# Optimization experiments

Hardware: AMD Instinct MI355X
Metric: run time of the kernel (lower is better)

## Reference

```python
import jax, jax.numpy as jnp
import numpy as np

B, N, DIM, H, HD, COND, BS = 2, 1024, 768, 12, 64, 128, 16
S = 2 * N  # noised tokens [0:N) concatenated with clean x0 tokens [N:2N)
EPS = 1e-5
NEG = -1e30


def setup_inputs() -> dict:
    key = jax.random.key(0)
    ks = jax.random.split(key, 8)
    d = {}
    d['x'] = jax.random.normal(ks[0], (B, S, DIM), jnp.float32)
    d['c'] = jax.random.normal(ks[1], (B, COND), jnp.float32)
    # Rotary table for positions 0..N-1 (each half of the 2N sequence reuses the same positions)
    inv_freq = 1.0 / (10000.0 ** (np.arange(0, HD, 2, dtype=np.float64) / HD))
    freqs = np.arange(N, dtype=np.float64)[:, None] * inv_freq[None, :]
    emb = np.concatenate([freqs, freqs], axis=-1)  # [N, HD]
    cos = np.tile(np.cos(emb), (2, 1))[None, :, None, None, :]
    sin = np.tile(np.sin(emb), (2, 1))[None, :, None, None, :]
    d['cos'] = jnp.asarray(cos, jnp.float32)
    d['sin'] = jnp.asarray(sin, jnp.float32)
    # block-causal diffusion mask (flex_attention_mask): same (block, x0-flag) OR
    # cross-attention from noised block q>0 to strictly earlier CLEAN (x0) blocks
    idx = np.arange(S)
    fl = (idx >= N).astype(np.int64)
    blk = np.where(fl == 1, (idx - N) // BS, idx // BS)
    same = (blk[:, None] == blk[None, :]) & (fl[:, None] == fl[None, :])
    allowed = (blk[:, None] > 0) & (blk[None, :] < blk[:, None]) & (fl[None, :] == 1)
    d['mask'] = jnp.asarray(same | allowed)
    # parameters (adaLN is zero-init in the source; randomized here so the block is non-trivial)
    w = 0.02
    d['norm1_w'] = jnp.ones((DIM,), jnp.float32)
    d['qkv_w'] = jax.random.normal(ks[2], (3 * DIM, DIM), jnp.float32) * w
    d['attn_out_w'] = jax.random.normal(ks[3], (DIM, DIM), jnp.float32) * w
    d['norm2_w'] = jnp.ones((DIM,), jnp.float32)
    d['mlp_w1'] = jax.random.normal(ks[4], (4 * DIM, DIM), jnp.float32) * w
    d['mlp_b1'] = jnp.zeros((4 * DIM,), jnp.float32)
    d['mlp_w2'] = jax.random.normal(ks[5], (DIM, 4 * DIM), jnp.float32) * w
    d['mlp_b2'] = jnp.zeros((DIM,), jnp.float32)
    d['adaLN_w'] = jax.random.normal(ks[6], (6 * DIM, COND), jnp.float32) * w
    d['adaLN_b'] = jax.random.normal(ks[7], (6 * DIM,), jnp.float32) * w
    return d


def _ln(x, w):
    # F.layer_norm (no bias) followed by learned scale, as in the custom LayerNorm
    mu = x.mean(-1, keepdims=True)
    xc = x - mu
    var = (xc * xc).mean(-1, keepdims=True)
    return xc * jax.lax.rsqrt(var + EPS) * w


def reference(x, c, cos, sin, mask, norm1_w, qkv_w, attn_out_w, norm2_w,
              mlp_w1, mlp_b1, mlp_w2, mlp_b2, adaLN_w, adaLN_b):
    # adaLN modulation: [B, 6*DIM] -> six [B, 1, DIM] chunks
    mods = c @ adaLN_w.T + adaLN_b
    (shift_msa, scale_msa, gate_msa,
     shift_mlp, scale_mlp, gate_mlp) = jnp.split(mods[:, None, :], 6, axis=-1)
    x_skip = x
    h = _ln(x, norm1_w) * (1.0 + scale_msa) + shift_msa  # modulate_fused
    # qkv projection + rotary (torchscript path: qkv*cos + rotate_half(qkv)*sin)
    qkv = (h @ qkv_w.T).reshape(x.shape[0], S, 3, H, HD)
    rot = jnp.concatenate([-qkv[..., HD // 2:], qkv[..., :HD // 2]], axis=-1)
    qkv = qkv * cos + rot * sin
    q, k, v = qkv[:, :, 0], qkv[:, :, 1], qkv[:, :, 2]
    # SDPA with the block-causal diffusion mask, scale 1/sqrt(head_dim)
    scores = jnp.einsum('bqhd,bkhd->bhqk', q, k) / np.sqrt(HD).astype(np.float32)
    scores = jnp.where(mask[None, None], scores, NEG)
    p = jax.nn.softmax(scores, axis=-1)
    a = jnp.einsum('bhqk,bkhd->bqhd', p, v).reshape(x.shape[0], S, DIM)
    # bias_dropout_add_scale (inference => no dropout): gate * attn_out + residual
    x = gate_msa * (a @ attn_out_w.T) + x_skip
    h2 = _ln(x, norm2_w) * (1.0 + scale_mlp) + shift_mlp
    m = jax.nn.gelu(h2 @ mlp_w1.T + mlp_b1, approximate=True) @ mlp_w2.T + mlp_b2
    return x + gate_mlp * m
```

## Files before the change

### kernel.cpp

```cpp
#include <hip/hip_runtime.h>
#include <hip/hip_bf16.h>

#define EPS 1e-5f

typedef __attribute__((ext_vector_type(8))) short bf16x8;
typedef __attribute__((ext_vector_type(4))) short bf16x4;
typedef __attribute__((ext_vector_type(4))) float f32x4;

__device__ __forceinline__ f32x4 mfma_bf16(bf16x8 a, bf16x8 b, f32x4 c) {
    return __builtin_amdgcn_mfma_f32_16x16x32_bf16(a, b, c, 0, 0, 0);
}

__device__ __forceinline__ void async_ld16(const void* g, void* l) {
    __builtin_amdgcn_global_load_lds(
        (const __attribute__((address_space(1))) void*)g,
        (__attribute__((address_space(3))) void*)l, 16, 0, 0);
}

__global__ void k_adaln(const float* __restrict__ c, const float* __restrict__ w,
                        const float* __restrict__ bias, float* __restrict__ mods) {
    int i = blockIdx.x * 256 + threadIdx.x;
    int b = i / 4608, row = i - b * 4608;
    const float4* cv = (const float4*)(c + b * 128);
    const float4* wv = (const float4*)(w + (long)row * 128);
    float acc = 0.f;
#pragma unroll
    for (int k = 0; k < 32; ++k) {
        float4 a = cv[k], bb = wv[k];
        acc += a.x * bb.x + a.y * bb.y + a.z * bb.z + a.w * bb.w;
    }
    mods[i] = acc + bias[row];
}

__global__ void k_f2b4(const float* __restrict__ a, __hip_bfloat16* __restrict__ oa, int na,
                       const float* __restrict__ b, __hip_bfloat16* __restrict__ ob, int nb,
                       const float* __restrict__ c, __hip_bfloat16* __restrict__ oc, int nc,
                       const float* __restrict__ d, __hip_bfloat16* __restrict__ od, int nd) {
    int i = blockIdx.x * 256 + threadIdx.x;
    if (i < na) { oa[i] = __float2bfloat16(a[i]); return; }
    i -= na;
    if (i < nb) { ob[i] = __float2bfloat16(b[i]); return; }
    i -= nb;
    if (i < nc) { oc[i] = __float2bfloat16(c[i]); return; }
    i -= nc;
    if (i < nd) od[i] = __float2bfloat16(d[i]);
}

__global__ void k_ln_mod(const float* __restrict__ x, const float* __restrict__ w,
                         const float* __restrict__ mods, int shiftOff, int scaleOff,
                         __hip_bfloat16* __restrict__ out) {
    int token = blockIdx.x;
    int lane = threadIdx.x;
    const float4* xr = (const float4*)(x + (long)token * 768);
    float4 v0 = xr[lane], v1 = xr[lane + 64], v2 = xr[lane + 128];
    float s  = v0.x + v0.y + v0.z + v0.w + v1.x + v1.y + v1.z + v1.w + v2.x + v2.y + v2.z + v2.w;
    float ss = v0.x*v0.x + v0.y*v0.y + v0.z*v0.z + v0.w*v0.w
             + v1.x*v1.x + v1.y*v1.y + v1.z*v1.z + v1.w*v1.w
             + v2.x*v2.x + v2.y*v2.y + v2.z*v2.z + v2.w*v2.w;
#pragma unroll
    for (int m = 32; m >= 1; m >>= 1) { s += __shfl_xor(s, m); ss += __shfl_xor(ss, m); }
    float mu = s * (1.f / 768.f);
    float var = ss * (1.f / 768.f) - mu * mu;
    float rs = rsqrtf(var + EPS);
    int b = token >> 11;
    const float* sh = mods + b * 4608 + shiftOff;
    const float* sc = mods + b * 4608 + scaleOff;
    __hip_bfloat16* o = out + (long)token * 768;
    float4 vv[3] = {v0, v1, v2};
#pragma unroll
    for (int kk = 0; kk < 3; ++kk) {
        int cbase = (lane + 64 * kk) * 4;
        const float* p = (const float*)&vv[kk];
#pragma unroll
        for (int j = 0; j < 4; ++j) {
            int col = cbase + j;
            float hv = (p[j] - mu) * rs * w[col] * (1.f + sc[col]) + sh[col];
            o[col] = __float2bfloat16(hv);
        }
    }
}

__global__ __launch_bounds__(256) void k_attn(
    const __hip_bfloat16* __restrict__ q, const __hip_bfloat16* __restrict__ k,
    const __hip_bfloat16* __restrict__ vT, __hip_bfloat16* __restrict__ out) {
    __shared__ __hip_bfloat16 pbuf[4][640];
    int wave = threadIdx.x >> 6;
    int lane = threadIdx.x & 63;
    int l15 = lane & 15, quad = lane >> 4;
    int bh = blockIdx.x >> 5;
    int pp = blockIdx.x & 31;
    int fl, blk;
    if      (wave == 0) { fl = 0; blk = 2 * pp; }
    else if (wave == 1) { fl = 0; blk = 2 * pp + 1; }
    else if (wave == 2) { fl = 1; blk = 63 - 2 * pp; }
    else                { fl = 1; blk = 62 - 2 * pp; }
    int qblk = fl * 64 + blk;

    const __hip_bfloat16* Q = q + ((long)bh * 2048 + qblk * 16) * 64;
    bf16x8 qa = *(const bf16x8*)(Q + l15 * 64 + quad * 8);
    bf16x8 qb = *(const bf16x8*)(Q + l15 * 64 + 32 + quad * 8);
    const __hip_bfloat16* K = k + (long)bh * 2048 * 64;
    const __hip_bfloat16* V = vT + (long)bh * 64 * 2048;
    __hip_bfloat16* P = &pbuf[wave][0];

    const f32x4 vzero = {0.f, 0.f, 0.f, 0.f};
    f32x4 o[4]; float l[4];
#pragma unroll
    for (int r = 0; r < 4; ++r) { o[r] = vzero; l[r] = 0.f; }

    int plen = (blk + fl) * 16;
    int nch = (plen + 31) >> 5;
    int total = nch + (fl ? 0 : 1);

    int kbase = (0 < nch) ? 1024 : blk * 16;
    bool v1 = (0 < nch) && (16 < plen);
    bf16x8 ka, kb, k1a, k1b;
    {
        const __hip_bfloat16* K0 = K + (long)kbase * 64;
        ka = *(const bf16x8*)(K0 + l15 * 64 + quad * 8);
        kb = *(const bf16x8*)(K0 + l15 * 64 + 32 + quad * 8);
        k1a = ka; k1b = kb;
        if (v1) {
            const __hip_bfloat16* K1 = K0 + 16 * 64;
            k1a = *(const bf16x8*)(K1 + l15 * 64 + quad * 8);
            k1b = *(const bf16x8*)(K1 + l15 * 64 + 32 + quad * 8);
        }
    }

    for (int ci = 0; ci < total; ++ci) {
        bf16x8 vf[4];
#pragma unroll
        for (int tt = 0; tt < 4; ++tt)
            vf[tt] = *(const bf16x8*)(V + (long)(tt * 16 + l15) * 2048 + kbase + quad * 8);

        f32x4 s0 = mfma_bf16(qb, kb, mfma_bf16(qa, ka, vzero));
        f32x4 s1 = vzero;
        if (v1) s1 = mfma_bf16(qb, k1b, mfma_bf16(qa, k1a, vzero));

        bool hasNext = (ci + 1) < total;
        int nkbase = kbase; bool nv1 = false;
        bf16x8 nka = ka, nkb = kb, nk1a = ka, nk1b = kb;
        if (hasNext) {
            nkbase = (ci + 1 < nch) ? 1024 + (ci + 1) * 32 : blk * 16;
            nv1 = (ci + 1 < nch) && ((ci + 1) * 32 + 16) < plen;
            const __hip_bfloat16* K0 = K + (long)nkbase * 64;
            nka = *(const bf16x8*)(K0 + l15 * 64 + quad * 8);
            nkb = *(const bf16x8*)(K0 + l15 * 64 + 32 + quad * 8);
            if (nv1) {
                const __hip_bfloat16* K1 = K0 + 16 * 64;
                nk1a = *(const bf16x8*)(K1 + l15 * 64 + quad * 8);
                nk1b = *(const bf16x8*)(K1 + l15 * 64 + 32 + quad * 8);
            }
        }

        float p0[4], p1[4];
#pragma unroll
        for (int r = 0; r < 4; ++r) p0[r] = __expf(s0[r]);
        if (v1) {
#pragma unroll
            for (int r = 0; r < 4; ++r) p1[r] = __expf(s1[r]);
        } else {
#pragma unroll
            for (int r = 0; r < 4; ++r) p1[r] = 0.f;
        }
#pragma unroll
        for (int r = 0; r < 4; ++r) {
            l[r] += p0[r] + p1[r];
            int row = quad * 4 + r;
            P[row * 36 + l15]      = __float2bfloat16(p0[r]);
            P[row * 36 + 16 + l15] = __float2bfloat16(p1[r]);
        }
        asm volatile("s_waitcnt lgkmcnt(0)" ::: "memory");
        union { bf16x4 h[2]; bf16x8 v; } u;
        u.h[0] = *(const bf16x4*)(P + l15 * 36 + quad * 8);
        u.h[1] = *(const bf16x4*)(P + l15 * 36 + quad * 8 + 4);
        bf16x8 pa = u.v;
#pragma unroll
        for (int tt = 0; tt < 4; ++tt) o[tt] = mfma_bf16(pa, vf[tt], o[tt]);
        asm volatile("s_waitcnt lgkmcnt(0)" ::: "memory");

        kbase = nkbase; v1 = nv1;
        ka = nka; kb = nkb; k1a = nk1a; k1b = nk1b;
    }

    int b = bh / 12, h = bh - b * 12;
    int seqbase = qblk * 16;
#pragma unroll
    for (int r = 0; r < 4; ++r) {
        float lr = l[r];
#pragma unroll
        for (int msk = 1; msk < 16; msk <<= 1) lr += __shfl_xor(lr, msk, 16);
        float inv = 1.f / lr;
        long row = b * 2048 + seqbase + quad * 4 + r;
#pragma unroll
        for (int tt = 0; tt < 4; ++tt)
            out[row * 768 + h * 64 + tt * 16 + l15] = __float2bfloat16(o[tt][r] * inv);
    }
}

template <int MODE, int TN>
__global__ __launch_bounds__(TN == 128 ? 256 : 128) void k_gemm(
    const __hip_bfloat16* __restrict__ A, const __hip_bfloat16* __restrict__ W,
    float* __restrict__ Cf, __hip_bfloat16* __restrict__ Cb,
    const float* __restrict__ bias, const float* __restrict__ mods, int gateOff,
    const float* __restrict__ resid, const float* __restrict__ cosb,
    const float* __restrict__ sinb, __hip_bfloat16* __restrict__ qo,
    __hip_bfloat16* __restrict__ ko, __hip_bfloat16* __restrict__ vo,
    int M, int N, int K) {
    constexpr int NW = (TN == 128) ? 4 : 2;
    constexpr int ACH = 512 / (NW * 64);
    constexpr int BCH = (TN * 4) / (NW * 64);
    constexpr int NINST = ACH + BCH;
    __shared__ __hip_bfloat16 lA[3][128 * 32];
    __shared__ __hip_bfloat16 lB[3][TN * 32];
    int t = threadIdx.x;
    int wave = t >> 6, lane = t & 63, l15 = lane & 15, quad = lane >> 4;
    int wr = (TN == 128) ? (wave >> 1) : wave;
    int wc = (TN == 128) ? (wave & 1) : 0;
    int sw8 = (quad ^ ((l15 >> 1) & 3)) * 8;
    long bm = blockIdx.x, bn = blockIdx.y;
    const __hip_bfloat16* Ab = A + bm * 128 * K;
    const __hip_bfloat16* Wb = W + bn * TN * K;

    long soffA[ACH], soffB[BCH];
#pragma unroll
    for (int cc = 0; cc < ACH; ++cc) {
        int chunk = cc * NW * 64 + t;
        int row = chunk >> 2;
        int c = (chunk & 3) ^ ((row >> 1) & 3);
        soffA[cc] = (long)row * K + c * 8;
    }
#pragma unroll
    for (int cc = 0; cc < BCH; ++cc) {
        int chunk = cc * NW * 64 + t;
        int row = chunk >> 2;
        int c = (chunk & 3) ^ ((row >> 1) & 3);
        soffB[cc] = (long)row * K + c * 8;
    }
    auto stage = [&](int k0, int buf) {
        char* lAc = (char*)&lA[buf][0];
        char* lBc = (char*)&lB[buf][0];
#pragma unroll
        for (int cc = 0; cc < ACH; ++cc)
            async_ld16(Ab + soffA[cc] + k0, lAc + cc * (NW * 1024) + wave * 1024);
#pragma unroll
        for (int cc = 0; cc < BCH; ++cc)
            async_ld16(Wb + soffB[cc] + k0, lBc + cc * (NW * 1024) + wave * 1024);
    };

    f32x4 acc[4][4];
#pragma unroll
    for (int i = 0; i < 4; ++i)
#pragma unroll
        for (int j = 0; j < 4; ++j) acc[i][j] = (f32x4){0.f, 0.f, 0.f, 0.f};

    int nIter = K / 32;
    stage(0, 0);
    stage(32, 1);
    int cb = 0;
    for (int i = 0; i < nIter; ++i) {
        if (i > 0) asm volatile("s_barrier" ::: "memory");
        if (i + 2 < nIter) {
            int nb = cb + 2; if (nb >= 3) nb -= 3;
            stage((i + 2) * 32, nb);
            asm volatile("s_waitcnt vmcnt(%0)" :: "n"(2 * NINST) : "memory");
        } else if (i + 2 == nIter) {
            asm volatile("s_waitcnt vmcnt(%0)" :: "n"(NINST) : "memory");
        } else {
            asm volatile("s_waitcnt vmcnt(0)" ::: "memory");
        }
        asm volatile("s_barrier" ::: "memory");
        bf16x8 af[4], bfr[4];
#pragma unroll
        for (int ii = 0; ii < 4; ++ii)
            af[ii] = *(const bf16x8*)&lA[cb][(wr * 64 + ii * 16 + l15) * 32 + sw8];
#pragma unroll
        for (int j = 0; j < 4; ++j)
            bfr[j] = *(const bf16x8*)&lB[cb][(wc * 64 + j * 16 + l15) * 32 + sw8];
#pragma unroll
        for (int ii = 0; ii < 4; ++ii)
#pragma unroll
            for (int j = 0; j < 4; ++j)
                acc[ii][j] = mfma_bf16(af[ii], bfr[j], acc[ii][j]);
        ++cb; if (cb >= 3) cb = 0;
    }

    if (MODE == 4) {
        int hcol = (int)bn * 2 + wc;
        int th = hcol / 12, h = hcol % 12;
#pragma unroll
        for (int i = 0; i < 4; ++i) {
#pragma unroll
            for (int r = 0; r < 4; ++r) {
                int row = (int)bm * 128 + wr * 64 + i * 16 + quad * 4 + r;
                int s = row & 2047, b = row >> 11;
                long bh_ = b * 12 + h;
                const float* cbp = cosb + s * 64;
                const float* sbp = sinb + s * 64;
#pragma unroll
                for (int j = 0; j < 2; ++j) {
                    int dh = j * 16 + l15;
                    float a0f = acc[i][j][r], a1f = acc[i][j + 2][r];
                    float o0 = a0f * cbp[dh] - a1f * sbp[dh];
                    float o1 = a1f * cbp[dh + 32] + a0f * sbp[dh + 32];
                    if (th == 0) {
                        __hip_bfloat16* d = qo + (bh_ * 2048 + s) * 64;
                        d[dh]      = __float2bfloat16(o0 * 0.125f);
                        d[dh + 32] = __float2bfloat16(o1 * 0.125f);
                    } else if (th == 1) {
                        __hip_bfloat16* d = ko + (bh_ * 2048 + s) * 64;
                        d[dh]      = __float2bfloat16(o0);
                        d[dh + 32] = __float2bfloat16(o1);
                    } else {
                        __hip_bfloat16* d = vo + bh_ * 64 * 2048 + s;
                        d[(long)dh * 2048]        = __float2bfloat16(o0);
                        d[(long)(dh + 32) * 2048] = __float2bfloat16(o1);
                    }
                }
            }
        }
        return;
    }

#pragma unroll
    for (int i = 0; i < 4; ++i) {
#pragma unroll
        for (int j = 0; j < 4; ++j) {
#pragma unroll
            for (int r = 0; r < 4; ++r) {
                int row = (int)bm * 128 + wr * 64 + i * 16 + quad * 4 + r;
                int col = (int)bn * TN + wc * 64 + j * 16 + l15;
                float v = acc[i][j][r];
                long idx = (long)row * N + col;
                if (MODE == 1) {
                    Cf[idx] = mods[(row >> 11) * 4608 + gateOff + col] * v + resid[idx];
                } else if (MODE == 2) {
                    v += bias[col];
                    float g = 0.5f * v * (1.f + tanhf(0.7978845608028654f * (v + 0.044715f * v * v * v)));
                    Cb[idx] = __float2bfloat16(g);
                } else {
                    Cf[idx] = resid[idx] + mods[(row >> 11) * 4608 + gateOff + col] * (v + bias[col]);
                }
            }
        }
    }
}

extern "C" void kernel_launch(void* const* d_in, const int* in_sizes, int n_in,
                              void* d_out, int out_size, void* d_ws, size_t ws_size,
                              hipStream_t stream) {
    const float* x    = (const float*)d_in[0];
    const float* c    = (const float*)d_in[1];
    const float* cosb = (const float*)d_in[2];
    const float* sinb = (const float*)d_in[3];
    const float* n1w  = (const float*)d_in[5];
    const float* qkvw = (const float*)d_in[6];
    const float* aow  = (const float*)d_in[7];
    const float* n2w  = (const float*)d_in[8];
    const float* w1   = (const float*)d_in[9];
    const float* b1   = (const float*)d_in[10];
    const float* w2   = (const float*)d_in[11];
    const float* b2   = (const float*)d_in[12];
    const float* alw  = (const float*)d_in[13];
    const float* alb  = (const float*)d_in[14];

    char* ws = (char*)d_ws;
    size_t off = 0;
    auto alloc = [&](size_t bytes) -> void* {
        void* p = ws + off;
        off += (bytes + 255) & ~(size_t)255;
        return p;
    };
    float*          mods = (float*)alloc(2 * 4608 * 4);
    __hip_bfloat16* hbuf = (__hip_bfloat16*)alloc((size_t)4096 * 768 * 2);
    __hip_bfloat16* qb   = (__hip_bfloat16*)alloc((size_t)24 * 2048 * 64 * 2);
    __hip_bfloat16* kb   = (__hip_bfloat16*)alloc((size_t)24 * 2048 * 64 * 2);
    __hip_bfloat16* vT   = (__hip_bfloat16*)alloc((size_t)24 * 64 * 2048 * 2);
    __hip_bfloat16* abuf = (__hip_bfloat16*)alloc((size_t)4096 * 768 * 2);
    float*          x2   = (float*)alloc((size_t)4096 * 768 * 4);
    __hip_bfloat16* h2   = (__hip_bfloat16*)alloc((size_t)4096 * 768 * 2);
    __hip_bfloat16* m1   = (__hip_bfloat16*)alloc((size_t)4096 * 3072 * 2);
    __hip_bfloat16* wq   = (__hip_bfloat16*)alloc((size_t)2304 * 768 * 2);
    __hip_bfloat16* wa   = (__hip_bfloat16*)alloc((size_t)768 * 768 * 2);
    __hip_bfloat16* w1b  = (__hip_bfloat16*)alloc((size_t)3072 * 768 * 2);
    __hip_bfloat16* w2b  = (__hip_bfloat16*)alloc((size_t)768 * 3072 * 2);

    k_adaln<<<36, 256, 0, stream>>>(c, alw, alb, mods);
    k_f2b4<<<27648, 256, 0, stream>>>(qkvw, wq, 2304 * 768, aow, wa, 768 * 768,
                                      w1, w1b, 3072 * 768, w2, w2b, 768 * 3072);
    k_ln_mod<<<4096, 64, 0, stream>>>(x, n1w, mods, 0, 768, hbuf);
    k_gemm<4, 128><<<dim3(32, 18), 256, 0, stream>>>(hbuf, wq, nullptr, nullptr, nullptr, nullptr, 0,
                                                     nullptr, cosb, sinb, qb, kb, vT,
                                                     4096, 2304, 768);
    k_attn<<<768, 256, 0, stream>>>(qb, kb, vT, abuf);
    k_gemm<1, 64><<<dim3(32, 12), 128, 0, stream>>>(abuf, wa, x2, nullptr, nullptr, mods, 1536,
                                                    x, nullptr, nullptr, nullptr, nullptr, nullptr,
                                                    4096, 768, 768);
    k_ln_mod<<<4096, 64, 0, stream>>>(x2, n2w, mods, 2304, 3072, h2);
    k_gemm<2, 128><<<dim3(32, 24), 256, 0, stream>>>(h2, w1b, nullptr, m1, b1, nullptr, 0,
                                                     nullptr, nullptr, nullptr, nullptr, nullptr, nullptr,
                                                     4096, 3072, 768);
    k_gemm<3, 64><<<dim3(32, 12), 128, 0, stream>>>(m1, w2b, (float*)d_out, nullptr, b2, mods, 3840,
                                                    x2, nullptr, nullptr, nullptr, nullptr, nullptr,
                                                    4096, 768, 3072);
}
```

Before: 332.1 us.

## Add 64x64 MLP-up GEMM with fast GELU, merge adaLN into weight cast

The MLP first-layer GEMM moves from the 128x128 templated kernel to a new 64x64-tile kernel with a 4-stage async LDS pipeline. This gives 3072 blocks instead of 768 for better CU occupancy and load balance. The tanh GELU is replaced by an exp-based sigmoid form, which is algebraically equivalent. The adaLN modulation GEMV is folded into the weight-conversion kernel as extra blocks, removing one launch. Smaller tiles give less data reuse per block.

```diff
diff --git a/kernel.cpp b/kernel.cpp
--- a/kernel.cpp
+++ b/kernel.cpp
@@ -17,25 +17,32 @@
         (__attribute__((address_space(3))) void*)l, 16, 0, 0);
 }
 
-__global__ void k_adaln(const float* __restrict__ c, const float* __restrict__ w,
-                        const float* __restrict__ bias, float* __restrict__ mods) {
-    int i = blockIdx.x * 256 + threadIdx.x;
-    int b = i / 4608, row = i - b * 4608;
-    const float4* cv = (const float4*)(c + b * 128);
-    const float4* wv = (const float4*)(w + (long)row * 128);
-    float acc = 0.f;
-#pragma unroll
-    for (int k = 0; k < 32; ++k) {
-        float4 a = cv[k], bb = wv[k];
-        acc += a.x * bb.x + a.y * bb.y + a.z * bb.z + a.w * bb.w;
-    }
-    mods[i] = acc + bias[row];
-}
-
-__global__ void k_f2b4(const float* __restrict__ a, __hip_bfloat16* __restrict__ oa, int na,
-                       const float* __restrict__ b, __hip_bfloat16* __restrict__ ob, int nb,
-                       const float* __restrict__ c, __hip_bfloat16* __restrict__ oc, int nc,
-                       const float* __restrict__ d, __hip_bfloat16* __restrict__ od, int nd) {
+__device__ __forceinline__ float fast_gelu(float v) {
+    float z2 = 1.5957691216057308f * (v + 0.044715f * v * v * v);
+    float e = __expf(z2);
+    return v * e / (e + 1.f);
+}
+
+__global__ void k_pre(const float* __restrict__ a, __hip_bfloat16* __restrict__ oa, int na,
+                      const float* __restrict__ b, __hip_bfloat16* __restrict__ ob, int nb,
+                      const float* __restrict__ c, __hip_bfloat16* __restrict__ oc, int nc,
+                      const float* __restrict__ d, __hip_bfloat16* __restrict__ od, int nd,
+                      const float* __restrict__ cond, const float* __restrict__ alw,
+                      const float* __restrict__ alb, float* __restrict__ mods) {
+    if (blockIdx.x >= 27648) {
+        int i = (blockIdx.x - 27648) * 256 + threadIdx.x;
+        int bb = i / 4608, row = i - bb * 4608;
+        const float4* cv = (const float4*)(cond + bb * 128);
+        const float4* wv = (const float4*)(alw + (long)row * 128);
+        float acc = 0.f;
+#pragma unroll
+        for (int k = 0; k < 32; ++k) {
+            float4 x = cv[k], y = wv[k];
+            acc += x.x * y.x + x.y * y.y + x.z * y.z + x.w * y.w;
+        }
+        mods[i] = acc + alb[row];
+        return;
+    }
     int i = blockIdx.x * 256 + threadIdx.x;
     if (i < na) { oa[i] = __float2bfloat16(a[i]); return; }
     i -= na;
@@ -195,6 +202,90 @@
 #pragma unroll
         for (int tt = 0; tt < 4; ++tt)
             out[row * 768 + h * 64 + tt * 16 + l15] = __float2bfloat16(o[tt][r] * inv);
+    }
+}
+
+__global__ __launch_bounds__(128) void k_gemm64(
+    const __hip_bfloat16* __restrict__ A, const __hip_bfloat16* __restrict__ W,
+    __hip_bfloat16* __restrict__ Cb, const float* __restrict__ bias,
+    int M, int N, int K) {
+    __shared__ __hip_bfloat16 lA[4][64 * 32];
+    __shared__ __hip_bfloat16 lB[4][64 * 32];
+    int t = threadIdx.x;
+    int wave = t >> 6, lane = t & 63, l15 = lane & 15, quad = lane >> 4;
+    int sw8 = (quad ^ ((l15 >> 1) & 3)) * 8;
+    long bm = blockIdx.x, bn = blockIdx.y;
+    const __hip_bfloat16* Ab = A + bm * 64 * K;
+    const __hip_bfloat16* Wb = W + bn * 64 * K;
+
+    long soff[2];
+#pragma unroll
+    for (int call = 0; call < 2; ++call) {
+        int chunk = call * 128 + t;
+        int row = chunk >> 2;
+        int c = (chunk & 3) ^ ((row >> 1) & 3);
+        soff[call] = (long)row * K + c * 8;
+    }
+    auto stage = [&](int k0, int buf) {
+        char* lAc = (char*)&lA[buf][0];
+        char* lBc = (char*)&lB[buf][0];
+#pragma unroll
+        for (int call = 0; call < 2; ++call) {
+            async_ld16(Ab + soff[call] + k0, lAc + call * 2048 + wave * 1024);
+            async_ld16(Wb + soff[call] + k0, lBc + call * 2048 + wave * 1024);
+        }
+    };
+
+    f32x4 acc[2][4];
+#pragma unroll
+    for (int i = 0; i < 2; ++i)
+#pragma unroll
+        for (int j = 0; j < 4; ++j) acc[i][j] = (f32x4){0.f, 0.f, 0.f, 0.f};
+
+    int nIter = K / 32;
+    stage(0, 0);
+    stage(32, 1);
+    stage(64, 2);
+    for (int i = 0; i < nIter; ++i) {
+        int cb = i & 3;
+        if (i > 0) asm volatile("s_barrier" ::: "memory");
+        if (i + 3 < nIter) {
+            stage((i + 3) * 32, (i + 3) & 3);
+            asm volatile("s_waitcnt vmcnt(12)" ::: "memory");
+        } else if (i + 3 == nIter) {
+            asm volatile("s_waitcnt vmcnt(8)" ::: "memory");
+        } else if (i + 2 == nIter) {
+            asm volatile("s_waitcnt vmcnt(4)" ::: "memory");
+        } else {
+            asm volatile("s_waitcnt vmcnt(0)" ::: "memory");
+        }
+        asm volatile("s_barrier" ::: "memory");
+        bf16x8 af[2], bfr[4];
+#pragma unroll
+        for (int ii = 0; ii < 2; ++ii)
+            af[ii] = *(const bf16x8*)&lA[cb][(wave * 32 + ii * 16 + l15) * 32 + sw8];
+#pragma unroll
+        for (int j = 0; j < 4; ++j)
+            bfr[j] = *(const bf16x8*)&lB[cb][(j * 16 + l15) * 32 + sw8];
+#pragma unroll
+        for (int ii = 0; ii < 2; ++ii)
+#pragma unroll
+            for (int j = 0; j < 4; ++j)
+                acc[ii][j] = mfma_bf16(af[ii], bfr[j], acc[ii][j]);
+    }
+
+#pragma unroll
+    for (int i = 0; i < 2; ++i) {
+#pragma unroll
+        for (int j = 0; j < 4; ++j) {
+#pragma unroll
+            for (int r = 0; r < 4; ++r) {
+                int row = (int)bm * 64 + wave * 32 + i * 16 + quad * 4 + r;
+                int col = (int)bn * 64 + j * 16 + l15;
+                float v = acc[i][j][r] + bias[col];
+                Cb[(long)row * N + col] = __float2bfloat16(fast_gelu(v));
+            }
+        }
     }
 }
 
@@ -334,10 +425,6 @@
                 long idx = (long)row * N + col;
                 if (MODE == 1) {
                     Cf[idx] = mods[(row >> 11) * 4608 + gateOff + col] * v + resid[idx];
-                } else if (MODE == 2) {
-                    v += bias[col];
-                    float g = 0.5f * v * (1.f + tanhf(0.7978845608028654f * (v + 0.044715f * v * v * v)));
-                    Cb[idx] = __float2bfloat16(g);
                 } else {
                     Cf[idx] = resid[idx] + mods[(row >> 11) * 4608 + gateOff + col] * (v + bias[col]);
                 }
@@ -385,9 +472,9 @@
     __hip_bfloat16* w1b  = (__hip_bfloat16*)alloc((size_t)3072 * 768 * 2);
     __hip_bfloat16* w2b  = (__hip_bfloat16*)alloc((size_t)768 * 3072 * 2);
 
-    k_adaln<<<36, 256, 0, stream>>>(c, alw, alb, mods);
-    k_f2b4<<<27648, 256, 0, stream>>>(qkvw, wq, 2304 * 768, aow, wa, 768 * 768,
-                                      w1, w1b, 3072 * 768, w2, w2b, 768 * 3072);
+    k_pre<<<27684, 256, 0, stream>>>(qkvw, wq, 2304 * 768, aow, wa, 768 * 768,
+                                     w1, w1b, 3072 * 768, w2, w2b, 768 * 3072,
+                                     c, alw, alb, mods);
     k_ln_mod<<<4096, 64, 0, stream>>>(x, n1w, mods, 0, 768, hbuf);
     k_gemm<4, 128><<<dim3(32, 18), 256, 0, stream>>>(hbuf, wq, nullptr, nullptr, nullptr, nullptr, 0,
                                                      nullptr, cosb, sinb, qb, kb, vT,
@@ -397,9 +484,7 @@
                                                     x, nullptr, nullptr, nullptr, nullptr, nullptr,
                                                     4096, 768, 768);
     k_ln_mod<<<4096, 64, 0, stream>>>(x2, n2w, mods, 2304, 3072, h2);
-    k_gemm<2, 128><<<dim3(32, 24), 256, 0, stream>>>(h2, w1b, nullptr, m1, b1, nullptr, 0,
-                                                     nullptr, nullptr, nullptr, nullptr, nullptr, nullptr,
-                                                     4096, 3072, 768);
+    k_gemm64<<<dim3(64, 48), 128, 0, stream>>>(h2, w1b, m1, b1, 4096, 3072, 768);
     k_gemm<3, 64><<<dim3(32, 12), 128, 0, stream>>>(m1, w2b, (float*)d_out, nullptr, b2, mods, 3840,
                                                     x2, nullptr, nullptr, nullptr, nullptr, nullptr,
                                                     4096, 768, 3072);
```

New measurement: 341.8 us. 2.9% more time.
